# Kernel tuning notes

Hardware: AMD Instinct MI355X
Metric: run time of the kernel (lower is better)

The kernel has to match this reference:

```python
import jax, jax.numpy as jnp
import numpy as np

C1 = 512  # channels1 (query input dim)
C = 512   # channels (model dim)


def setup_inputs() -> dict:
    key = jax.random.key(0)
    ks = jax.random.split(key, 12)
    B, Lq, Lk = 8, 2048, 2048
    s1 = 1.0 / np.sqrt(C1)
    s = 1.0 / np.sqrt(C)
    return {
        "rep": jax.random.normal(ks[0], (B, Lq, C1), dtype=jnp.float32),
        "rep1": jax.random.normal(ks[1], (B, Lk, C), dtype=jnp.float32),
        "Wq_w": jax.random.uniform(ks[2], (C1, C), jnp.float32, -s1, s1),
        "Wq_b": jax.random.uniform(ks[3], (C,), jnp.float32, -s1, s1),
        "Wk_w": jax.random.uniform(ks[4], (C, C), jnp.float32, -s, s),
        "Wk_b": jax.random.uniform(ks[5], (C,), jnp.float32, -s, s),
        "Wv_w": jax.random.uniform(ks[6], (C, C), jnp.float32, -s, s),
        "Wv_b": jax.random.uniform(ks[7], (C,), jnp.float32, -s, s),
        "FC_w": jax.random.uniform(ks[8], (C, C), jnp.float32, -s, s),
        "FC_b": jax.random.uniform(ks[9], (C,), jnp.float32, -s, s),
    }


def reference(rep, rep1, Wq_w, Wq_b, Wk_w, Wk_b, Wv_w, Wv_b, FC_w, FC_b):
    # Linear + ReLU projections (single head)
    q = jax.nn.relu(jnp.einsum('blc,cd->bld', rep, Wq_w) + Wq_b)    # [B,Lq,C]
    k = jax.nn.relu(jnp.einsum('blc,cd->bld', rep1, Wk_w) + Wk_b)   # [B,Lk,C]
    v = jax.nn.relu(jnp.einsum('blc,cd->bld', rep1, Wv_w) + Wv_b)   # [B,Lk,C]
    scores = jnp.einsum('bqd,bkd->bqk', q, k) / jnp.sqrt(jnp.float32(C))
    attn = jax.nn.softmax(scores, axis=-1)                           # [B,Lq,Lk]
    out = jnp.einsum('bqk,bkd->bqd', attn, v)                        # [B,Lq,C]
    out = jax.nn.relu(jnp.einsum('bld,de->ble', out, FC_w) + FC_b)
    return out
```

## Files before the change

### kernel.cpp

```cpp
#include <hip/hip_runtime.h>


typedef __attribute__((ext_vector_type(8))) short short8;
typedef __attribute__((ext_vector_type(4))) float f32x4;

#define SEQ 2048
#define CH 512
#define NB 8
#define MTOT (NB * SEQ)

#define GLDS16(gp, lp)                                                                  \
  __builtin_amdgcn_global_load_lds((const __attribute__((address_space(1))) void*)(gp), \
                                   (__attribute__((address_space(3))) void*)(lp), 16, 0, 0)

__device__ __forceinline__ unsigned short f2bf(float f) {
  unsigned u = __float_as_uint(f);
  u += 0x7fffu + ((u >> 16) & 1u);
  return (unsigned short)(u >> 16);
}

__global__ __launch_bounds__(256) void prep_kernel(
    const float* __restrict__ rep, const float* __restrict__ rep1,
    unsigned short* __restrict__ repb, unsigned short* __restrict__ rep1b,
    const float* __restrict__ W0, const float* __restrict__ W1,
    const float* __restrict__ W2, const float* __restrict__ W3,
    unsigned short* __restrict__ Wt,
    const float* __restrict__ Wk_b, const float* __restrict__ Wv_b,
    float* __restrict__ biasKV, float* __restrict__ rowsum) {
  __shared__ __attribute__((aligned(16))) unsigned short tile[64 * 72];
  const int blk = blockIdx.x;
  const int t = threadIdx.x;
  if (blk < 8192) {
    const float* in = (blk < 4096) ? rep : rep1;
    unsigned short* out = (blk < 4096) ? repb : rep1b;
    long i = ((long)(blk & 4095) * 256 + t) * 8;
    float4 a = *(const float4*)(in + i);
    float4 b = *(const float4*)(in + i + 4);
    ushort4 o0, o1;
    o0.x = f2bf(a.x); o0.y = f2bf(a.y); o0.z = f2bf(a.z); o0.w = f2bf(a.w);
    o1.x = f2bf(b.x); o1.y = f2bf(b.y); o1.z = f2bf(b.z); o1.w = f2bf(b.w);
    *(ushort4*)(out + i) = o0;
    *(ushort4*)(out + i + 4) = o1;
  } else if (blk < 8448) {
    const int zz = blk - 8192;
    const int z = zz >> 6;
    const int bx = zz & 7, by = (zz >> 3) & 7;
    const float* W = (z == 0) ? W0 : (z == 1) ? W1 : (z == 2) ? W2 : W3;
    unsigned short* Wtz = Wt + (long)z * 512 * 512;
    const int k0 = by * 64, n0 = bx * 64;
    const int r = t >> 4, cq = (t & 15) * 4;
#pragma unroll
    for (int j = 0; j < 4; ++j) {
      int row = r + 16 * j;
      float4 v = *(const float4*)&W[(long)(k0 + row) * 512 + n0 + cq];
      tile[row * 72 + cq + 0] = f2bf(v.x);
      tile[row * 72 + cq + 1] = f2bf(v.y);
      tile[row * 72 + cq + 2] = f2bf(v.z);
      tile[row * 72 + cq + 3] = f2bf(v.w);
    }
    __syncthreads();
#pragma unroll
    for (int j = 0; j < 4; ++j) {
      int row = r + 16 * j;
      ushort4 o;
      o.x = tile[(cq + 0) * 72 + row];
      o.y = tile[(cq + 1) * 72 + row];
      o.z = tile[(cq + 2) * 72 + row];
      o.w = tile[(cq + 3) * 72 + row];
      *(ushort4*)&Wtz[(long)(n0 + row) * 512 + k0 + cq] = o;
    }
  } else if (blk == 8448) {
    biasKV[t] = Wk_b[t];
    biasKV[t + 256] = Wk_b[t + 256];
    biasKV[t + 512] = Wv_b[t];
    biasKV[t + 768] = Wv_b[t + 256];
  } else {
    const int zb = blk - 8449;
    f32x4 z4 = {0.f, 0.f, 0.f, 0.f};
    *(f32x4*)&rowsum[(zb * 256 + t) * 4] = z4;
  }
}

template <int EPI, int LDA, int LDB, int LDO, int K, int BK>
__device__ __forceinline__ void gemm_body(const unsigned short* __restrict__ A,
                                          const unsigned short* __restrict__ Bt,
                                          const float* __restrict__ bias,
                                          float* __restrict__ rowsum,
                                          void* __restrict__ outp,
                                          long m0, long n0, unsigned short* smem) {
  unsigned short* Al = smem;
  unsigned short* Bl = smem + 128 * BK;
  const int t = threadIdx.x;
  const int w = t >> 6, l = t & 63;
  const int wr = w >> 1, wc = w & 1;
  const int lr = l & 15, lg = l >> 4;
  constexpr int NC = BK / 8;
  const int rl = l / NC, cc0 = l % NC;
  unsigned short* la = &Al[32 * w * BK];
  unsigned short* lb = &Bl[32 * w * BK];
  const int srow = 32 * w + rl;
  const int sxor = (cc0 ^ (rl & (NC - 1))) * 8;
  const unsigned short* ga = A + (m0 + srow) * (long)LDA + sxor;
  const unsigned short* gb = Bt + (n0 + srow) * (long)LDB + sxor;

  f32x4 acc[4][4] = {};
  for (int k0 = 0; k0 < K; k0 += BK) {
#pragma unroll
    for (int j = 0; j < 4; ++j) {
      GLDS16(ga + (long)8 * j * LDA, la + j * 8 * BK);
      GLDS16(gb + (long)8 * j * LDB, lb + j * 8 * BK);
    }
    ga += BK; gb += BK;
    __syncthreads();
#pragma unroll
    for (int h = 0; h < BK / 32; ++h) {
      short8 af[4], bfr[4];
#pragma unroll
      for (int i = 0; i < 4; ++i) {
        const int kc = ((h * 4 + lg) ^ (lr & (NC - 1))) * 8;
        af[i]  = *(short8*)&Al[(64 * wr + 16 * i + lr) * BK + kc];
        bfr[i] = *(short8*)&Bl[(64 * wc + 16 * i + lr) * BK + kc];
      }
#pragma unroll
      for (int mi = 0; mi < 4; ++mi)
#pragma unroll
        for (int ni = 0; ni < 4; ++ni)
          acc[mi][ni] =
              __builtin_amdgcn_mfma_f32_16x16x32_bf16(af[mi], bfr[ni], acc[mi][ni], 0, 0, 0);
    }
    __syncthreads();
  }

  if (EPI == 1 || EPI == 6 || EPI == 2) {
    unsigned short* patch = smem;
    float bv[4];
    if (EPI == 1) {
#pragma unroll
      for (int ni = 0; ni < 4; ++ni) bv[ni] = bias[n0 + 64 * wc + 16 * ni + lr];
    }
    float rsum[4][4] = {};
#pragma unroll
    for (int mi = 0; mi < 4; ++mi)
#pragma unroll
      for (int ni = 0; ni < 4; ++ni)
#pragma unroll
        for (int r = 0; r < 4; ++r) {
          const int m = 64 * wr + 16 * mi + 4 * lg + r;
          const int n = 64 * wc + 16 * ni + lr;
          float a = acc[mi][ni][r];
          unsigned short ob;
          if (EPI == 1)      ob = f2bf(fmaxf(a + bv[ni], 0.0f));
          else if (EPI == 6) ob = f2bf(a);
          else {
            float p = exp2f(a * 0.06375872f);
            ob = f2bf(p);
            rsum[mi][r] += __uint_as_float((unsigned)ob << 16);
          }
          patch[m * 128 + ((n >> 3) ^ (m & 15)) * 8 + (n & 7)] = ob;
        }
    __syncthreads();
    unsigned short* O = (unsigned short*)outp;
    const int q = t & 3;
#pragma unroll
    for (int p = 0; p < 2; ++p) {
      const int m = 64 * p + (t >> 2);
#pragma unroll
      for (int i = 0; i < 4; ++i) {
        const int cc = i * 4 + q;
        short8 x = *(short8*)&patch[m * 128 + ((cc ^ (m & 15)) * 8)];
        *(short8*)&O[(m0 + m) * LDO + n0 + cc * 8] = x;
      }
    }
    if (EPI == 2) {
#pragma unroll
      for (int off = 1; off < 16; off <<= 1)
#pragma unroll
        for (int mi = 0; mi < 4; ++mi)
#pragma unroll
          for (int r = 0; r < 4; ++r) rsum[mi][r] += __shfl_xor(rsum[mi][r], off);
      if (lr == 0) {
#pragma unroll
        for (int mi = 0; mi < 4; ++mi)
#pragma unroll
          for (int r = 0; r < 4; ++r)
            atomicAdd(&rowsum[m0 + 64 * wr + 16 * mi + 4 * lg + r], rsum[mi][r]);
      }
    }
  } else {
    float* patchF = (float*)smem;
    float bv[4];
#pragma unroll
    for (int ni = 0; ni < 4; ++ni) bv[ni] = bias[n0 + 64 * wc + 16 * ni + lr];
    float inv[4][4];
#pragma unroll
    for (int mi = 0; mi < 4; ++mi)
#pragma unroll
      for (int r = 0; r < 4; ++r)
        inv[mi][r] = 1.0f / rowsum[m0 + 64 * wr + 16 * mi + 4 * lg + r];
#pragma unroll
    for (int mi = 0; mi < 4; ++mi)
#pragma unroll
      for (int ni = 0; ni < 4; ++ni)
#pragma unroll
        for (int r = 0; r < 4; ++r) {
          const int m = 64 * wr + 16 * mi + 4 * lg + r;
          const int n = 64 * wc + 16 * ni + lr;
          patchF[m * 128 + ((n >> 2) ^ (m & 31)) * 4 + (n & 3)] =
              fmaxf(acc[mi][ni][r] * inv[mi][r] + bv[ni], 0.0f);
        }
    __syncthreads();
    float* O = (float*)outp;
    const int q = t & 3;
#pragma unroll
    for (int p = 0; p < 2; ++p) {
      const int m = 64 * p + (t >> 2);
#pragma unroll
      for (int i = 0; i < 8; ++i) {
        const int cc = i * 4 + q;
        f32x4 x = *(f32x4*)&patchF[m * 128 + ((cc ^ (m & 31)) * 4)];
        *(f32x4*)&O[(m0 + m) * LDO + n0 + cc * 4] = x;
      }
    }
  }
}

template <int EPI, int LDA, int LDB, int LDO, int K, int BK>
__global__ __launch_bounds__(256) void gemm_nt(const unsigned short* __restrict__ A, long sAb,
                                               const unsigned short* __restrict__ Bt, long sBb,
                                               const float* __restrict__ bias,
                                               float* __restrict__ rowsum, long sRb,
                                               void* __restrict__ outp, long sOb) {
  constexpr int SM = (EPI == 5) ? 32768 : 2 * 128 * BK;
  __shared__ __attribute__((aligned(16))) unsigned short smem[SM];
  const int bz = blockIdx.z;
  void* o = (EPI == 5) ? (void*)((float*)outp + (long)bz * sOb)
                       : (void*)((unsigned short*)outp + (long)bz * sOb);
  float* rs = rowsum ? rowsum + (long)bz * sRb : nullptr;
  gemm_body<EPI, LDA, LDB, LDO, K, BK>(A + (long)bz * sAb, Bt + (long)bz * sBb, bias, rs, o,
                                       (long)blockIdx.y * 128, (long)blockIdx.x * 128, smem);
}

__global__ __launch_bounds__(256) void proj_kernel(const unsigned short* __restrict__ repb,
                                                   const unsigned short* __restrict__ rep1b,
                                                   const unsigned short* __restrict__ Wt,
                                                   const float* __restrict__ Wq_b,
                                                   const float* __restrict__ biasKV,
                                                   unsigned short* __restrict__ Qb,
                                                   unsigned short* __restrict__ KVb) {
  __shared__ __attribute__((aligned(16))) unsigned short smem[2 * 128 * 64];
  const long m0 = (long)blockIdx.y * 128;
  if (blockIdx.x < 4) {
    gemm_body<1, CH, CH, CH, CH, 64>(repb, Wt, Wq_b, nullptr, Qb, m0,
                                     (long)blockIdx.x * 128, smem);
  } else {
    gemm_body<1, CH, CH, 1024, CH, 64>(rep1b, Wt + 512 * 512, biasKV, nullptr, KVb, m0,
                                       (long)(blockIdx.x - 4) * 128, smem);
  }
}

extern "C" void kernel_launch(void* const* d_in, const int* in_sizes, int n_in,
                              void* d_out, int out_size, void* d_ws, size_t ws_size,
                              hipStream_t stream) {
  const float* rep  = (const float*)d_in[0];
  const float* rep1 = (const float*)d_in[1];
  const float* Wq_w = (const float*)d_in[2];
  const float* Wq_b = (const float*)d_in[3];
  const float* Wk_w = (const float*)d_in[4];
  const float* Wk_b = (const float*)d_in[5];
  const float* Wv_w = (const float*)d_in[6];
  const float* Wv_b = (const float*)d_in[7];
  const float* FC_w = (const float*)d_in[8];
  const float* FC_b = (const float*)d_in[9];
  float* out = (float*)d_out;
  char* ws = (char*)d_ws;

  const size_t MB = 1024 * 1024;
  unsigned short* Qb     = (unsigned short*)(ws + 0 * MB);
  unsigned short* KVb    = (unsigned short*)(ws + 16 * MB);
  unsigned short* repb   = (unsigned short*)(ws + 48 * MB);
  unsigned short* rep1b  = (unsigned short*)(ws + 64 * MB);
  unsigned short* Wt4    = (unsigned short*)(ws + 80 * MB);
  float*          biasKV = (float*)(ws + 82 * MB);
  unsigned short* Pbuf   = (unsigned short*)(ws + 83 * MB);
  float*          rowsum = (float*)(ws + 147 * MB);
  const size_t need = 148 * MB;
  if (ws_size < need) return;

  unsigned short* WtQ = Wt4;
  unsigned short* WtF = Wt4 + 3 * 512 * 512;
  unsigned short* VFt = repb;

  prep_kernel<<<8465, 256, 0, stream>>>(rep, rep1, repb, rep1b, Wq_w, Wk_w, Wv_w, FC_w,
                                        Wt4, Wk_b, Wv_b, biasKV, rowsum);

  proj_kernel<<<dim3(12, 128), 256, 0, stream>>>(repb, rep1b, Wt4, Wq_b, biasKV, Qb, KVb);

  gemm_nt<6, CH, 1024, SEQ, CH, 64><<<dim3(16, 4, 8), 256, 0, stream>>>(
      WtF, 0, KVb + 512, (long)SEQ * 1024, nullptr, nullptr, 0, VFt, (long)CH * SEQ);

  gemm_nt<2, CH, 1024, SEQ, CH, 64><<<dim3(16, 16, 8), 256, 0, stream>>>(
      Qb, (long)SEQ * CH, KVb, (long)SEQ * 1024, nullptr, rowsum, SEQ,
      Pbuf, (long)SEQ * SEQ);

  gemm_nt<5, SEQ, SEQ, CH, SEQ, 64><<<dim3(4, 16, 8), 256, 0, stream>>>(
      Pbuf, (long)SEQ * SEQ, VFt, (long)CH * SEQ, FC_b, rowsum, SEQ,
      (void*)out, (long)SEQ * CH);
}
```

Baseline: 296.7 us.

## Fuse fp32-to-bf16 input conversion into projection GEMM and merge QK/VF launches

The separate pass that converted rep and rep1 to bf16 is removed. The projection kernel now loads fp32 activations straight into LDS and packs them to bf16 (by truncation via perm) while building MFMA fragments. The V·FC GEMM and the QK^T/exp GEMM are also merged into one launch by extending the grid's y dimension. This drops a full read/write round trip of the inputs and one kernel launch. In exchange the projection uses a smaller K tile of 32, and rounding changes from round-to-nearest to truncation.

```diff
diff --git a/kernel.cpp b/kernel.cpp
--- a/kernel.cpp
+++ b/kernel.cpp
@@ -19,9 +19,11 @@
   return (unsigned short)(u >> 16);
 }
 
-__global__ __launch_bounds__(256) void prep_kernel(
-    const float* __restrict__ rep, const float* __restrict__ rep1,
-    unsigned short* __restrict__ repb, unsigned short* __restrict__ rep1b,
+__device__ __forceinline__ unsigned pack2bf(float lo, float hi) {
+  return __builtin_amdgcn_perm(__float_as_uint(hi), __float_as_uint(lo), 0x07060302u);
+}
+
+__global__ __launch_bounds__(256) void prep2_kernel(
     const float* __restrict__ W0, const float* __restrict__ W1,
     const float* __restrict__ W2, const float* __restrict__ W3,
     unsigned short* __restrict__ Wt,
@@ -30,21 +32,9 @@
   __shared__ __attribute__((aligned(16))) unsigned short tile[64 * 72];
   const int blk = blockIdx.x;
   const int t = threadIdx.x;
-  if (blk < 8192) {
-    const float* in = (blk < 4096) ? rep : rep1;
-    unsigned short* out = (blk < 4096) ? repb : rep1b;
-    long i = ((long)(blk & 4095) * 256 + t) * 8;
-    float4 a = *(const float4*)(in + i);
-    float4 b = *(const float4*)(in + i + 4);
-    ushort4 o0, o1;
-    o0.x = f2bf(a.x); o0.y = f2bf(a.y); o0.z = f2bf(a.z); o0.w = f2bf(a.w);
-    o1.x = f2bf(b.x); o1.y = f2bf(b.y); o1.z = f2bf(b.z); o1.w = f2bf(b.w);
-    *(ushort4*)(out + i) = o0;
-    *(ushort4*)(out + i + 4) = o1;
-  } else if (blk < 8448) {
-    const int zz = blk - 8192;
-    const int z = zz >> 6;
-    const int bx = zz & 7, by = (zz >> 3) & 7;
+  if (blk < 256) {
+    const int z = blk >> 6;
+    const int bx = blk & 7, by = (blk >> 3) & 7;
     const float* W = (z == 0) ? W0 : (z == 1) ? W1 : (z == 2) ? W2 : W3;
     unsigned short* Wtz = Wt + (long)z * 512 * 512;
     const int k0 = by * 64, n0 = bx * 64;
@@ -69,16 +59,108 @@
       o.w = tile[(cq + 3) * 72 + row];
       *(ushort4*)&Wtz[(long)(n0 + row) * 512 + k0 + cq] = o;
     }
-  } else if (blk == 8448) {
+  } else if (blk == 256) {
     biasKV[t] = Wk_b[t];
     biasKV[t + 256] = Wk_b[t + 256];
     biasKV[t + 512] = Wv_b[t];
     biasKV[t + 768] = Wv_b[t + 256];
   } else {
-    const int zb = blk - 8449;
+    const int zb = blk - 257;
     f32x4 z4 = {0.f, 0.f, 0.f, 0.f};
     *(f32x4*)&rowsum[(zb * 256 + t) * 4] = z4;
   }
+}
+
+template <int LDO>
+__device__ __forceinline__ void proj_body(const float* __restrict__ A,
+                                          const unsigned short* __restrict__ Bt,
+                                          const float* __restrict__ bias,
+                                          unsigned short* __restrict__ Op,
+                                          long m0, long n0, unsigned short* smem) {
+  float* Af = (float*)smem;
+  unsigned short* Bl = smem + 8192;
+  const int t = threadIdx.x;
+  const int w = t >> 6, l = t & 63;
+  const int wr = w >> 1, wc = w & 1;
+  const int lr = l & 15, lg = l >> 4;
+  const float* ga = A + (m0 + 32 * w + (l >> 3)) * CH + ((l & 7) ^ (l >> 3)) * 4;
+  const unsigned short* gb =
+      Bt + (n0 + 32 * w + (l >> 2)) * CH + (((l & 3) ^ ((l >> 3) & 3)) * 8);
+  float* la = Af + 32 * w * 32;
+  unsigned short* lb = Bl + 32 * w * 32;
+
+  f32x4 acc[4][4] = {};
+  for (int k0 = 0; k0 < CH; k0 += 32) {
+#pragma unroll
+    for (int j = 0; j < 4; ++j) GLDS16(ga + 8 * j * CH, la + 8 * j * 32);
+    GLDS16(gb, lb);
+    GLDS16(gb + 16 * CH, lb + 16 * 32);
+    ga += 32; gb += 32;
+    __syncthreads();
+    short8 af[4], bfr[4];
+#pragma unroll
+    for (int i = 0; i < 4; ++i) {
+      const int row = 64 * wr + 16 * i + lr;
+      f32x4 a0 = *(f32x4*)&Af[row * 32 + ((2 * lg) ^ (lr & 7)) * 4];
+      f32x4 a1 = *(f32x4*)&Af[row * 32 + ((2 * lg + 1) ^ (lr & 7)) * 4];
+      union { unsigned u[4]; short8 s; } pk;
+      pk.u[0] = pack2bf(a0[0], a0[1]);
+      pk.u[1] = pack2bf(a0[2], a0[3]);
+      pk.u[2] = pack2bf(a1[0], a1[1]);
+      pk.u[3] = pack2bf(a1[2], a1[3]);
+      af[i] = pk.s;
+      bfr[i] = *(short8*)&Bl[(64 * wc + 16 * i + lr) * 32 + (lg ^ ((lr >> 1) & 3)) * 8];
+    }
+#pragma unroll
+    for (int mi = 0; mi < 4; ++mi)
+#pragma unroll
+      for (int ni = 0; ni < 4; ++ni)
+        acc[mi][ni] =
+            __builtin_amdgcn_mfma_f32_16x16x32_bf16(af[mi], bfr[ni], acc[mi][ni], 0, 0, 0);
+    __syncthreads();
+  }
+  unsigned short* patch = smem;
+  float bv[4];
+#pragma unroll
+  for (int ni = 0; ni < 4; ++ni) bv[ni] = bias[n0 + 64 * wc + 16 * ni + lr];
+#pragma unroll
+  for (int mi = 0; mi < 4; ++mi)
+#pragma unroll
+    for (int ni = 0; ni < 4; ++ni)
+#pragma unroll
+      for (int r = 0; r < 4; ++r) {
+        const int m = 64 * wr + 16 * mi + 4 * lg + r;
+        const int n = 64 * wc + 16 * ni + lr;
+        patch[m * 128 + ((n >> 3) ^ (m & 15)) * 8 + (n & 7)] =
+            f2bf(fmaxf(acc[mi][ni][r] + bv[ni], 0.0f));
+      }
+  __syncthreads();
+  const int q = t & 3;
+#pragma unroll
+  for (int p = 0; p < 2; ++p) {
+    const int m = 64 * p + (t >> 2);
+#pragma unroll
+    for (int i = 0; i < 4; ++i) {
+      const int cc = i * 4 + q;
+      short8 x = *(short8*)&patch[m * 128 + ((cc ^ (m & 15)) * 8)];
+      *(short8*)&Op[(m0 + m) * LDO + n0 + cc * 8] = x;
+    }
+  }
+}
+
+__global__ __launch_bounds__(256) void proj_kernel(const float* __restrict__ rep,
+                                                   const float* __restrict__ rep1,
+                                                   const unsigned short* __restrict__ Wt,
+                                                   const float* __restrict__ Wq_b,
+                                                   const float* __restrict__ biasKV,
+                                                   unsigned short* __restrict__ Qb,
+                                                   unsigned short* __restrict__ KVb) {
+  __shared__ __attribute__((aligned(16))) unsigned short smem[16384];
+  const long m0 = (long)blockIdx.y * 128;
+  if (blockIdx.x < 4)
+    proj_body<CH>(rep, Wt, Wq_b, Qb, m0, (long)blockIdx.x * 128, smem);
+  else
+    proj_body<1024>(rep1, Wt + 512 * 512, biasKV, KVb, m0, (long)(blockIdx.x - 4) * 128, smem);
 }
 
 template <int EPI, int LDA, int LDB, int LDO, int K, int BK>
@@ -131,13 +213,8 @@
     __syncthreads();
   }
 
-  if (EPI == 1 || EPI == 6 || EPI == 2) {
+  if (EPI == 6 || EPI == 2) {
     unsigned short* patch = smem;
-    float bv[4];
-    if (EPI == 1) {
-#pragma unroll
-      for (int ni = 0; ni < 4; ++ni) bv[ni] = bias[n0 + 64 * wc + 16 * ni + lr];
-    }
     float rsum[4][4] = {};
 #pragma unroll
     for (int mi = 0; mi < 4; ++mi)
@@ -149,8 +226,7 @@
           const int n = 64 * wc + 16 * ni + lr;
           float a = acc[mi][ni][r];
           unsigned short ob;
-          if (EPI == 1)      ob = f2bf(fmaxf(a + bv[ni], 0.0f));
-          else if (EPI == 6) ob = f2bf(a);
+          if (EPI == 6) ob = f2bf(a);
           else {
             float p = exp2f(a * 0.06375872f);
             ob = f2bf(p);
@@ -224,38 +300,38 @@
   }
 }
 
-template <int EPI, int LDA, int LDB, int LDO, int K, int BK>
-__global__ __launch_bounds__(256) void gemm_nt(const unsigned short* __restrict__ A, long sAb,
-                                               const unsigned short* __restrict__ Bt, long sBb,
-                                               const float* __restrict__ bias,
-                                               float* __restrict__ rowsum, long sRb,
-                                               void* __restrict__ outp, long sOb) {
-  constexpr int SM = (EPI == 5) ? 32768 : 2 * 128 * BK;
-  __shared__ __attribute__((aligned(16))) unsigned short smem[SM];
+__global__ __launch_bounds__(256) void qkvf_kernel(const unsigned short* __restrict__ Qb,
+                                                   const unsigned short* __restrict__ KVb,
+                                                   const unsigned short* __restrict__ WtF,
+                                                   float* __restrict__ rowsum,
+                                                   unsigned short* __restrict__ Pbuf,
+                                                   unsigned short* __restrict__ VFt) {
+  __shared__ __attribute__((aligned(16))) unsigned short smem[2 * 128 * 64];
   const int bz = blockIdx.z;
-  void* o = (EPI == 5) ? (void*)((float*)outp + (long)bz * sOb)
-                       : (void*)((unsigned short*)outp + (long)bz * sOb);
-  float* rs = rowsum ? rowsum + (long)bz * sRb : nullptr;
-  gemm_body<EPI, LDA, LDB, LDO, K, BK>(A + (long)bz * sAb, Bt + (long)bz * sBb, bias, rs, o,
-                                       (long)blockIdx.y * 128, (long)blockIdx.x * 128, smem);
-}
-
-__global__ __launch_bounds__(256) void proj_kernel(const unsigned short* __restrict__ repb,
-                                                   const unsigned short* __restrict__ rep1b,
-                                                   const unsigned short* __restrict__ Wt,
-                                                   const float* __restrict__ Wq_b,
-                                                   const float* __restrict__ biasKV,
-                                                   unsigned short* __restrict__ Qb,
-                                                   unsigned short* __restrict__ KVb) {
-  __shared__ __attribute__((aligned(16))) unsigned short smem[2 * 128 * 64];
-  const long m0 = (long)blockIdx.y * 128;
-  if (blockIdx.x < 4) {
-    gemm_body<1, CH, CH, CH, CH, 64>(repb, Wt, Wq_b, nullptr, Qb, m0,
-                                     (long)blockIdx.x * 128, smem);
+  if (blockIdx.y < 16) {
+    gemm_body<2, CH, 1024, SEQ, CH, 64>(
+        Qb + (long)bz * SEQ * CH, KVb + (long)bz * SEQ * 1024, nullptr,
+        rowsum + (long)bz * SEQ, Pbuf + (long)bz * SEQ * SEQ,
+        (long)blockIdx.y * 128, (long)blockIdx.x * 128, smem);
   } else {
-    gemm_body<1, CH, CH, 1024, CH, 64>(rep1b, Wt + 512 * 512, biasKV, nullptr, KVb, m0,
-                                       (long)(blockIdx.x - 4) * 128, smem);
-  }
+    gemm_body<6, CH, 1024, SEQ, CH, 64>(
+        WtF, KVb + 512 + (long)bz * SEQ * 1024, nullptr, nullptr,
+        VFt + (long)bz * CH * SEQ,
+        (long)(blockIdx.y - 16) * 128, (long)blockIdx.x * 128, smem);
+  }
+}
+
+__global__ __launch_bounds__(256) void pvf_kernel(const unsigned short* __restrict__ Pbuf,
+                                                  const unsigned short* __restrict__ VFt,
+                                                  const float* __restrict__ FC_b,
+                                                  float* __restrict__ rowsum,
+                                                  float* __restrict__ out) {
+  __shared__ __attribute__((aligned(16))) unsigned short smem[32768];
+  const int bz = blockIdx.z;
+  gemm_body<5, SEQ, SEQ, CH, SEQ, 64>(
+      Pbuf + (long)bz * SEQ * SEQ, VFt + (long)bz * CH * SEQ, FC_b,
+      rowsum + (long)bz * SEQ, out + (long)bz * SEQ * CH,
+      (long)blockIdx.y * 128, (long)blockIdx.x * 128, smem);
 }
 
 extern "C" void kernel_launch(void* const* d_in, const int* in_sizes, int n_in,
@@ -277,32 +353,22 @@
   const size_t MB = 1024 * 1024;
   unsigned short* Qb     = (unsigned short*)(ws + 0 * MB);
   unsigned short* KVb    = (unsigned short*)(ws + 16 * MB);
-  unsigned short* repb   = (unsigned short*)(ws + 48 * MB);
-  unsigned short* rep1b  = (unsigned short*)(ws + 64 * MB);
-  unsigned short* Wt4    = (unsigned short*)(ws + 80 * MB);
-  float*          biasKV = (float*)(ws + 82 * MB);
-  unsigned short* Pbuf   = (unsigned short*)(ws + 83 * MB);
-  float*          rowsum = (float*)(ws + 147 * MB);
-  const size_t need = 148 * MB;
+  unsigned short* VFt    = (unsigned short*)(ws + 48 * MB);
+  unsigned short* Wt4    = (unsigned short*)(ws + 64 * MB);
+  float*          biasKV = (float*)(ws + 66 * MB);
+  unsigned short* Pbuf   = (unsigned short*)(ws + 67 * MB);
+  float*          rowsum = (float*)(ws + 131 * MB);
+  const size_t need = 132 * MB;
   if (ws_size < need) return;
 
-  unsigned short* WtQ = Wt4;
   unsigned short* WtF = Wt4 + 3 * 512 * 512;
-  unsigned short* VFt = repb;
-
-  prep_kernel<<<8465, 256, 0, stream>>>(rep, rep1, repb, rep1b, Wq_w, Wk_w, Wv_w, FC_w,
-                                        Wt4, Wk_b, Wv_b, biasKV, rowsum);
-
-  proj_kernel<<<dim3(12, 128), 256, 0, stream>>>(repb, rep1b, Wt4, Wq_b, biasKV, Qb, KVb);
-
-  gemm_nt<6, CH, 1024, SEQ, CH, 64><<<dim3(16, 4, 8), 256, 0, stream>>>(
-      WtF, 0, KVb + 512, (long)SEQ * 1024, nullptr, nullptr, 0, VFt, (long)CH * SEQ);
-
-  gemm_nt<2, CH, 1024, SEQ, CH, 64><<<dim3(16, 16, 8), 256, 0, stream>>>(
-      Qb, (long)SEQ * CH, KVb, (long)SEQ * 1024, nullptr, rowsum, SEQ,
-      Pbuf, (long)SEQ * SEQ);
-
-  gemm_nt<5, SEQ, SEQ, CH, SEQ, 64><<<dim3(4, 16, 8), 256, 0, stream>>>(
-      Pbuf, (long)SEQ * SEQ, VFt, (long)CH * SEQ, FC_b, rowsum, SEQ,
-      (void*)out, (long)SEQ * CH);
-}
+
+  prep2_kernel<<<273, 256, 0, stream>>>(Wq_w, Wk_w, Wv_w, FC_w, Wt4, Wk_b, Wv_b,
+                                        biasKV, rowsum);
+
+  proj_kernel<<<dim3(12, 128), 256, 0, stream>>>(rep, rep1, Wt4, Wq_b, biasKV, Qb, KVb);
+
+  qkvf_kernel<<<dim3(16, 20, 8), 256, 0, stream>>>(Qb, KVb, WtF, rowsum, Pbuf, VFt);
+
+  pvf_kernel<<<dim3(4, 16, 8), 256, 0, stream>>>(Pbuf, VFt, FC_b, rowsum, out);
+}
```

Result: no change. 295.7 us (-0.3%).
